# Performance work log

Hardware: AMD Instinct MI355X
Metric: run time of the kernel (lower is better)

The kernel has to match this reference:

```python
import jax, jax.numpy as jnp
import numpy as np

N = 8192
N_DIM = 7
N_WIDTH = 64


def setup_inputs() -> dict:
    key = jax.random.key(0)
    ks = jax.random.split(key, 12)
    scale = 0.05
    u = lambda k, shape: scale * (2.0 * jax.random.uniform(k, shape) - 1.0)
    # Linear params stored as (in, out) so forward uses x @ W + b (same math as torch Linear).
    lin = lambda k, fan_in, fan_out: (
        jax.random.uniform(jax.random.fold_in(k, 0), (fan_in, fan_out),
                           minval=-1.0, maxval=1.0) / np.sqrt(fan_in),
        jax.random.uniform(jax.random.fold_in(k, 1), (fan_out,),
                           minval=-1.0, maxval=1.0) / np.sqrt(fan_in),
    )
    W1, b1 = lin(ks[1], N_DIM, N_WIDTH)
    W2, b2 = lin(ks[2], N_WIDTH, N_WIDTH)
    Wl, bl = lin(ks[3], N_WIDTH, 1)
    return {
        "x": jax.random.normal(ks[0], (N, N_DIM), dtype=jnp.float32),
        "alpha": jax.random.uniform(ks[4], (1,)),          # Edges.alpha = 1 * rand(1)
        "W1": W1, "b1": b1, "wt1": u(ks[5], (N_WIDTH, N_WIDTH)), "bs1": u(ks[6], (1,)),
        "W2": W2, "b2": b2, "wt2": u(ks[7], (N_WIDTH, N_WIDTH)), "bs2": u(ks[8], (1,)),
        "Wl": Wl, "bl": bl,
    }


def _edges(x, alpha):
    eta, phi = x[:, 1], x[:, 2]
    deta = eta[:, None] - eta[None, :]                      # (n, n)
    dphi = jnp.abs(phi[:, None] - phi[None, :])
    dphi = jnp.where(dphi > jnp.pi, 2.0 * jnp.pi - dphi, dphi)
    dRdR = deta * deta + dphi * dphi
    A = jnp.exp(-alpha[0] * dRdR)
    return jax.nn.softmax(A, axis=1) + jnp.eye(x.shape[0], dtype=x.dtype)


def _gcn_layer(X, A, W, b, wt, bs):
    X = jax.nn.relu(X @ W + b)                              # embed + relu
    X = (A @ X) @ wt + bs[0]                                # aggregate + mix + scalar bias
    return jax.nn.relu(X)


def reference(x, alpha, W1, b1, wt1, bs1, W2, b2, wt2, bs2, Wl, bl):
    A = _edges(x, alpha)
    V = jax.nn.relu(_gcn_layer(x, A, W1, b1, wt1, bs1))
    V = jax.nn.relu(_gcn_layer(V, A, W2, b2, wt2, bs2))
    s = V.sum(axis=0)                                       # (n_width,)
    return jax.nn.sigmoid(s @ Wl + bl)                      # (1,)
```

## Files before the change

### kernel.cpp

```cpp
#include <hip/hip_runtime.h>
#include <math.h>

#define NN 8192
#define L2E 1.44269504088896340736f
#define TWO_PI 6.28318530717958647693f

typedef _Float16 h8 __attribute__((ext_vector_type(8)));
typedef _Float16 h4 __attribute__((ext_vector_type(4)));
typedef float f32x4 __attribute__((ext_vector_type(4)));
#define MFMA16(A, B, C) __builtin_amdgcn_mfma_f32_16x16x32_f16(A, B, C, 0, 0, 0)

#define GLD_LDS16(gsrc, ldst)                                          \
  __builtin_amdgcn_global_load_lds(                                    \
      (const __attribute__((address_space(1))) unsigned int*)(gsrc),   \
      (__attribute__((address_space(3))) unsigned int*)(ldst), 16, 0, 0)

union V8 { float4 v[2]; float f[8]; };

__global__ __launch_bounds__(256) void prep_kernel(
    const float* __restrict__ x, const float* __restrict__ alpha,
    const float* __restrict__ W1, const float* __restrict__ b1,
    float* __restrict__ eta_s, float* __restrict__ phi_s,
    float* __restrict__ H1, _Float16* __restrict__ HT1,
    float* __restrict__ svec)
{
  __shared__ float sW[448];
  __shared__ float sb[64];
  __shared__ float T[32][65];
  const int t = threadIdx.x;
  if (blockIdx.x == 0 && t < 64) svec[t] = 0.f;
  for (int k = t; k < 448; k += 256) sW[k] = W1[k];
  if (t < 64) sb[t] = b1[t];
  const float s = sqrtf(alpha[0] * L2E);
  const int i0 = blockIdx.x * 32;
  const int r = t >> 3, q = t & 7;
  const int i = i0 + r;
  float xv[7];
#pragma unroll
  for (int k = 0; k < 7; k++) xv[k] = x[i * 7 + k];
  if (q == 0) { eta_s[i] = xv[1] * s; phi_s[i] = xv[2] * s; }
  __syncthreads();
#pragma unroll
  for (int c = 0; c < 8; c++) {
    const int n = q * 8 + c;
    float hv = sb[n];
#pragma unroll
    for (int k = 0; k < 7; k++) hv = fmaf(xv[k], sW[k * 64 + n], hv);
    T[r][n] = fmaxf(hv, 0.f);
  }
  __syncthreads();
  for (int e = t; e < 2048; e += 256) H1[i0 * 64 + e] = T[e >> 6][e & 63];
  const int n = t >> 2, sg = (t & 3) * 8;
  h8 v;
#pragma unroll
  for (int ss = 0; ss < 8; ss++) v[ss] = (_Float16)T[sg + ss][n];
  *(h8*)(HT1 + (size_t)n * NN + i0 + sg) = v;
}

template <bool NEED_L>
__global__ __launch_bounds__(256, 4) void attn_pass(
    const float* __restrict__ eta_s, const float* __restrict__ phi_s,
    const _Float16* __restrict__ HT, const float* __restrict__ alpha,
    float* __restrict__ Ypart, float* __restrict__ lpart)
{
  __shared__ __align__(16) char smem[33792];
  _Float16* stage = (_Float16*)smem;
  const int tid = threadIdx.x;
  const int w = tid >> 6, lane = tid & 63, m = lane & 15, g = lane >> 4;
  const int tile = blockIdx.x >> 2, part = blockIdx.x & 3;
  const int i0 = tile << 5;
  const int jbase = part << 11;
  const float Cs = TWO_PI * sqrtf(alpha[0] * L2E);
  const float et0 = eta_s[i0 + m],      ph0 = phi_s[i0 + m];
  const float et1 = eta_s[i0 + 16 + m], ph1 = phi_s[i0 + 16 + m];

  const int r0 = tid >> 4, gq = tid & 15;
  const _Float16* sbase = HT + (size_t)r0 * NN + ((gq ^ r0) << 3) + jbase;

  f32x4 a00 = {0,0,0,0}, a01 = {0,0,0,0}, a02 = {0,0,0,0}, a03 = {0,0,0,0};
  f32x4 a10 = {0,0,0,0}, a11 = {0,0,0,0}, a12 = {0,0,0,0}, a13 = {0,0,0,0};
  float l0 = 0.f, l1 = 0.f;

  const float* ep = eta_s + jbase + (w << 5) + (g << 3);
  const float* pp = phi_s + jbase + (w << 5) + (g << 3);
  V8 E, P, En, Pn;
  E.v[0] = *(const float4*)ep;  E.v[1] = *(const float4*)(ep + 4);
  P.v[0] = *(const float4*)pp;  P.v[1] = *(const float4*)(pp + 4);
  En = E; Pn = P;

#pragma unroll
  for (int k = 0; k < 4; ++k)
    GLD_LDS16(sbase + (size_t)k * 16 * NN, stage + ((k * 256 + tid) << 3));
  __syncthreads();

  const int fs = ((m << 4) + (((w << 2) | g) ^ m)) << 3;

  union AF { h8 v; decltype(__builtin_amdgcn_cvt_pkrtz(0.f, 0.f)) p[4]; };

  for (int s = 0; s < 16; ++s) {
    _Float16* cur = stage + ((s & 1) << 13);
    if (s < 15) {
      _Float16* nxt = stage + (((s + 1) & 1) << 13);
      const _Float16* srcp = sbase + (s + 1) * 128;
#pragma unroll
      for (int k = 0; k < 4; ++k)
        GLD_LDS16(srcp + (size_t)k * 16 * NN, nxt + ((k * 256 + tid) << 3));
      En.v[0] = *(const float4*)(ep + 128); En.v[1] = *(const float4*)(ep + 132);
      Pn.v[0] = *(const float4*)(pp + 128); Pn.v[1] = *(const float4*)(pp + 132);
      ep += 128; pp += 128;
    }
    const h8 b0 = *(const h8*)(cur + fs);
    const h8 b1 = *(const h8*)(cur + 2048 + fs);
    const h8 b2 = *(const h8*)(cur + 4096 + fs);
    const h8 b3 = *(const h8*)(cur + 6144 + fs);

    AF af0, af1;
#pragma unroll
    for (int tt = 0; tt < 8; tt += 2) {
      float Pv[4];
#pragma unroll
      for (int u = 0; u < 2; ++u) {
        {
          const float dp = ph0 - P.f[tt + u];
          const float ad = fabsf(dp);
          const float wr = fminf(ad, Cs - ad);
          const float de = et0 - E.f[tt + u];
          const float r2 = fmaf(de, de, wr * wr);
          const float a  = __builtin_amdgcn_exp2f(-r2);
          const float pv = __builtin_amdgcn_exp2f(fmaf(a, L2E, -L2E));
          if constexpr (NEED_L) l0 += pv;
          Pv[u] = pv;
        }
        {
          const float dp = ph1 - P.f[tt + u];
          const float ad = fabsf(dp);
          const float wr = fminf(ad, Cs - ad);
          const float de = et1 - E.f[tt + u];
          const float r2 = fmaf(de, de, wr * wr);
          const float a  = __builtin_amdgcn_exp2f(-r2);
          const float pv = __builtin_amdgcn_exp2f(fmaf(a, L2E, -L2E));
          if constexpr (NEED_L) l1 += pv;
          Pv[2 + u] = pv;
        }
      }
      af0.p[tt >> 1] = __builtin_amdgcn_cvt_pkrtz(Pv[0], Pv[1]);
      af1.p[tt >> 1] = __builtin_amdgcn_cvt_pkrtz(Pv[2], Pv[3]);
    }
    a00 = MFMA16(af0.v, b0, a00); a01 = MFMA16(af0.v, b1, a01);
    a02 = MFMA16(af0.v, b2, a02); a03 = MFMA16(af0.v, b3, a03);
    a10 = MFMA16(af1.v, b0, a10); a11 = MFMA16(af1.v, b1, a11);
    a12 = MFMA16(af1.v, b2, a12); a13 = MFMA16(af1.v, b3, a13);
    E = En; P = Pn;
    __syncthreads();
  }

  typedef float Red2[32][66];
  Red2* red = (Red2*)smem;
  float* lredF = (float*)(smem + 32768);
  const int h = w >> 1;
  if ((w & 1) == 0) {
#pragma unroll
    for (int r = 0; r < 4; ++r) {
      red[h][g * 4 + r][m]      = a00[r]; red[h][g * 4 + r][16 + m] = a01[r];
      red[h][g * 4 + r][32 + m] = a02[r]; red[h][g * 4 + r][48 + m] = a03[r];
      red[h][16 + g * 4 + r][m]      = a10[r]; red[h][16 + g * 4 + r][16 + m] = a11[r];
      red[h][16 + g * 4 + r][32 + m] = a12[r]; red[h][16 + g * 4 + r][48 + m] = a13[r];
    }
    if constexpr (NEED_L) {
      lredF[h * 128 + g * 32 + m] = l0; lredF[h * 128 + g * 32 + 16 + m] = l1;
    }
  }
  __syncthreads();
  if (w & 1) {
#pragma unroll
    for (int r = 0; r < 4; ++r) {
      red[h][g * 4 + r][m]      += a00[r]; red[h][g * 4 + r][16 + m] += a01[r];
      red[h][g * 4 + r][32 + m] += a02[r]; red[h][g * 4 + r][48 + m] += a03[r];
      red[h][16 + g * 4 + r][m]      += a10[r]; red[h][16 + g * 4 + r][16 + m] += a11[r];
      red[h][16 + g * 4 + r][32 + m] += a12[r]; red[h][16 + g * 4 + r][48 + m] += a13[r];
    }
    if constexpr (NEED_L) {
      lredF[h * 128 + g * 32 + m] += l0; lredF[h * 128 + g * 32 + 16 + m] += l1;
    }
  }
  __syncthreads();
#pragma unroll
  for (int k = 0; k < 8; ++k) {
    const int e = tid + k * 256;
    Ypart[((size_t)part * NN + i0 + (e >> 6)) * 64 + (e & 63)] =
        red[0][e >> 6][e & 63] + red[1][e >> 6][e & 63];
  }
  if constexpr (NEED_L) {
    if (tid < 32) {
      float sv = 0.f;
#pragma unroll
      for (int hh = 0; hh < 2; ++hh)
#pragma unroll
        for (int gg = 0; gg < 4; ++gg) sv += lredF[hh * 128 + gg * 32 + tid];
      lpart[(size_t)part * NN + i0 + tid] = sv;
    }
  }
}

__global__ __launch_bounds__(256) void mid_kernel(
    const float* __restrict__ Yp, const float* __restrict__ lp,
    const float* __restrict__ H1, const float* __restrict__ wt1,
    const float* __restrict__ bs1, const float* __restrict__ W2,
    const float* __restrict__ b2, float* __restrict__ H2,
    _Float16* __restrict__ HT2)
{
  __shared__ float sA[64][68];
  __shared__ float sB[64][68];
  __shared__ float U[16][65];
  __shared__ float sb2v[64];
  const int t = threadIdx.x;
  for (int e = t; e < 4096; e += 256) {
    sA[e >> 6][e & 63] = wt1[e];
    sB[e >> 6][e & 63] = W2[e];
  }
  if (t < 64) sb2v[t] = b2[t];
  const float bsv = bs1[0];
  const int i0 = blockIdx.x * 16;
  const int r = t >> 4, q = t & 15;
  const int i = i0 + r;
  float l = 0.f;
#pragma unroll
  for (int p = 0; p < 4; ++p) l += lp[(size_t)p * NN + i];
  const float rl = 1.0f / l;
  f32x4 ya = {0, 0, 0, 0};
#pragma unroll
  for (int p = 0; p < 4; ++p)
    ya += *(const f32x4*)(Yp + ((size_t)p * NN + i) * 64 + q * 4);
  const f32x4 h1 = *(const f32x4*)(H1 + (size_t)i * 64 + q * 4);
#pragma unroll
  for (int c = 0; c < 4; ++c) U[r][q * 4 + c] = fmaf(ya[c], rl, h1[c]);
  __syncthreads();
  float z[4];
#pragma unroll
  for (int c = 0; c < 4; ++c) z[c] = bsv;
  for (int k = 0; k < 64; ++k) {
    const float uk = U[r][k];
    const f32x4 sa = *(const f32x4*)&sA[k][q * 4];
#pragma unroll
    for (int c = 0; c < 4; ++c) z[c] = fmaf(uk, sa[c], z[c]);
  }
  __syncthreads();
#pragma unroll
  for (int c = 0; c < 4; ++c) U[r][q * 4 + c] = fmaxf(z[c], 0.f);
  __syncthreads();
  float hv[4];
#pragma unroll
  for (int c = 0; c < 4; ++c) hv[c] = sb2v[q * 4 + c];
  for (int k = 0; k < 64; ++k) {
    const float uk = U[r][k];
    const f32x4 sb4 = *(const f32x4*)&sB[k][q * 4];
#pragma unroll
    for (int c = 0; c < 4; ++c) hv[c] = fmaf(uk, sb4[c], hv[c]);
  }
  __syncthreads();
#pragma unroll
  for (int c = 0; c < 4; ++c) U[r][q * 4 + c] = fmaxf(hv[c], 0.f);
  __syncthreads();
  for (int e = t; e < 1024; e += 256) H2[i0 * 64 + e] = U[e >> 6][e & 63];
  const int n = t >> 2, sg = (t & 3) * 4;
  h4 v;
#pragma unroll
  for (int ss = 0; ss < 4; ss++) v[ss] = (_Float16)U[sg + ss][n];
  *(h4*)(HT2 + (size_t)n * NN + i0 + sg) = v;
}

__global__ __launch_bounds__(256) void final_kernel(
    const float* __restrict__ Yp, const float* __restrict__ lp,
    const float* __restrict__ H2, const float* __restrict__ wt2,
    const float* __restrict__ bs2, float* __restrict__ svec)
{
  __shared__ float sA[64][68];
  __shared__ float U[16][65];
  __shared__ float cred[4][64];
  const int t = threadIdx.x;
  for (int e = t; e < 4096; e += 256) sA[e >> 6][e & 63] = wt2[e];
  const float bsv = bs2[0];
  const int i0 = blockIdx.x * 16;
  const int r = t >> 4, q = t & 15;
  const int i = i0 + r;
  float l = 0.f;
#pragma unroll
  for (int p = 0; p < 4; ++p) l += lp[(size_t)p * NN + i];
  const float rl = 1.0f / l;
  f32x4 ya = {0, 0, 0, 0};
#pragma unroll
  for (int p = 0; p < 4; ++p)
    ya += *(const f32x4*)(Yp + ((size_t)p * NN + i) * 64 + q * 4);
  const f32x4 h2 = *(const f32x4*)(H2 + (size_t)i * 64 + q * 4);
#pragma unroll
  for (int c = 0; c < 4; ++c) U[r][q * 4 + c] = fmaf(ya[c], rl, h2[c]);
  __syncthreads();
  float z[4];
#pragma unroll
  for (int c = 0; c < 4; ++c) z[c] = bsv;
  for (int k = 0; k < 64; ++k) {
    const float uk = U[r][k];
    const f32x4 sa = *(const f32x4*)&sA[k][q * 4];
#pragma unroll
    for (int c = 0; c < 4; ++c) z[c] = fmaf(uk, sa[c], z[c]);
  }
  __syncthreads();
#pragma unroll
  for (int c = 0; c < 4; ++c) U[r][q * 4 + c] = fmaxf(z[c], 0.f);
  __syncthreads();
  const int col = t & 63, rg = t >> 6;
  float ps = 0.f;
#pragma unroll
  for (int rr = 0; rr < 4; rr++) ps += U[rg * 4 + rr][col];
  cred[rg][col] = ps;
  __syncthreads();
  if (t < 64)
    atomicAdd(svec + t, cred[0][t] + cred[1][t] + cred[2][t] + cred[3][t]);
}

__global__ void out_kernel(const float* __restrict__ svec,
                           const float* __restrict__ Wl,
                           const float* __restrict__ bl,
                           float* __restrict__ out)
{
  const int t = threadIdx.x;
  float v = svec[t] * Wl[t];
#pragma unroll
  for (int off = 32; off > 0; off >>= 1) v += __shfl_down(v, off);
  if (t == 0) {
    const float logit = v + bl[0];
    out[0] = 1.0f / (1.0f + __builtin_amdgcn_exp2f(-logit * L2E));
  }
}

extern "C" void kernel_launch(void* const* d_in, const int* in_sizes, int n_in,
                              void* d_out, int out_size, void* d_ws,
                              size_t ws_size, hipStream_t stream)
{
  const float* x     = (const float*)d_in[0];
  const float* alpha = (const float*)d_in[1];
  const float* W1    = (const float*)d_in[2];
  const float* b1    = (const float*)d_in[3];
  const float* wt1   = (const float*)d_in[4];
  const float* bs1   = (const float*)d_in[5];
  const float* W2    = (const float*)d_in[6];
  const float* b2    = (const float*)d_in[7];
  const float* wt2   = (const float*)d_in[8];
  const float* bs2   = (const float*)d_in[9];
  const float* Wl    = (const float*)d_in[10];
  const float* bl    = (const float*)d_in[11];
  float* out = (float*)d_out;

  char* ws = (char*)d_ws;
  size_t off = 0;
  auto alloc = [&](size_t bytes) {
    void* p = ws + off;
    off = (off + bytes + 255) & ~(size_t)255;
    return p;
  };
  float* eta_s = (float*)alloc(NN * 4 + 256);
  float* phi_s = (float*)alloc(NN * 4 + 256);
  float* H1    = (float*)alloc((size_t)NN * 64 * 4);
  float* H2    = (float*)alloc((size_t)NN * 64 * 4);
  float* Ypart = (float*)alloc((size_t)4 * NN * 64 * 4);
  float* lpart = (float*)alloc((size_t)4 * NN * 4);
  _Float16* HT = (_Float16*)alloc((size_t)NN * 64 * 2 + 512);
  float* svec  = (float*)alloc(64 * 4);

  prep_kernel<<<256, 256, 0, stream>>>(x, alpha, W1, b1, eta_s, phi_s, H1, HT, svec);
  attn_pass<true><<<1024, 256, 0, stream>>>(eta_s, phi_s, HT, alpha, Ypart, lpart);
  mid_kernel<<<512, 256, 0, stream>>>(Ypart, lpart, H1, wt1, bs1, W2, b2, H2, HT);
  attn_pass<false><<<1024, 256, 0, stream>>>(eta_s, phi_s, HT, alpha, Ypart, nullptr);
  final_kernel<<<512, 256, 0, stream>>>(Ypart, lpart, H2, wt2, bs2, svec);
  out_kernel<<<1, 64, 0, stream>>>(svec, Wl, bl, out);
}
```

Measured before the change: 170.6 us.

## Fuse attention passes with per-row epilogues and drop split-K partials

Restructures each attention pass so a 512-thread block owns 16 rows across the full j range, reducing over its 8 waves in LDS instead of writing four Ypart partials. The mid/final dense layers and the final sigmoid (via a last-block atomic ticket) are folded into the same kernels, removing three launches and the partial-sum round-trip through global memory. The trade-offs are larger LDS use (64KB), half as many blocks per pass, and a serial epilogue tail inside each block.

```diff
diff --git a/kernel.cpp b/kernel.cpp
--- a/kernel.cpp
+++ b/kernel.cpp
@@ -6,7 +6,6 @@
 #define TWO_PI 6.28318530717958647693f
 
 typedef _Float16 h8 __attribute__((ext_vector_type(8)));
-typedef _Float16 h4 __attribute__((ext_vector_type(4)));
 typedef float f32x4 __attribute__((ext_vector_type(4)));
 #define MFMA16(A, B, C) __builtin_amdgcn_mfma_f32_16x16x32_f16(A, B, C, 0, 0, 0)
 
@@ -16,6 +15,7 @@
       (__attribute__((address_space(3))) unsigned int*)(ldst), 16, 0, 0)
 
 union V8 { float4 v[2]; float f[8]; };
+union AF { h8 v; decltype(__builtin_amdgcn_cvt_pkrtz(0.f, 0.f)) p[4]; };
 
 __global__ __launch_bounds__(256) void prep_kernel(
     const float* __restrict__ x, const float* __restrict__ alpha,
@@ -57,32 +57,46 @@
   *(h8*)(HT1 + (size_t)n * NN + i0 + sg) = v;
 }
 
-template <bool NEED_L>
-__global__ __launch_bounds__(256, 4) void attn_pass(
+template <int PASS>
+__global__ __launch_bounds__(512, 4) void fused_pass(
     const float* __restrict__ eta_s, const float* __restrict__ phi_s,
-    const _Float16* __restrict__ HT, const float* __restrict__ alpha,
-    float* __restrict__ Ypart, float* __restrict__ lpart)
+    const _Float16* __restrict__ HTin, const float* __restrict__ Hres,
+    const float* __restrict__ WA, const float* __restrict__ bsA,
+    const float* __restrict__ WB, const float* __restrict__ bB,
+    const float* __restrict__ alpha, float* __restrict__ lsum,
+    float* __restrict__ Hout, _Float16* __restrict__ HTout,
+    float* __restrict__ svec, const float* __restrict__ Wl,
+    const float* __restrict__ bl, float* __restrict__ out,
+    unsigned* __restrict__ bar)
 {
-  __shared__ __align__(16) char smem[33792];
+  __shared__ __align__(16) char smem[65536];
+  __shared__ unsigned last_ticket;
   _Float16* stage = (_Float16*)smem;
   const int tid = threadIdx.x;
   const int w = tid >> 6, lane = tid & 63, m = lane & 15, g = lane >> 4;
-  const int tile = blockIdx.x >> 2, part = blockIdx.x & 3;
-  const int i0 = tile << 5;
-  const int jbase = part << 11;
+  const int i0 = blockIdx.x << 4;
   const float Cs = TWO_PI * sqrtf(alpha[0] * L2E);
-  const float et0 = eta_s[i0 + m],      ph0 = phi_s[i0 + m];
-  const float et1 = eta_s[i0 + 16 + m], ph1 = phi_s[i0 + 16 + m];
-
-  const int r0 = tid >> 4, gq = tid & 15;
-  const _Float16* sbase = HT + (size_t)r0 * NN + ((gq ^ r0) << 3) + jbase;
-
-  f32x4 a00 = {0,0,0,0}, a01 = {0,0,0,0}, a02 = {0,0,0,0}, a03 = {0,0,0,0};
-  f32x4 a10 = {0,0,0,0}, a11 = {0,0,0,0}, a12 = {0,0,0,0}, a13 = {0,0,0,0};
-  float l0 = 0.f, l1 = 0.f;
-
-  const float* ep = eta_s + jbase + (w << 5) + (g << 3);
-  const float* pp = phi_s + jbase + (w << 5) + (g << 3);
+  const float et0 = eta_s[i0 + m], ph0 = phi_s[i0 + m];
+
+  const int rr = tid >> 5, gq = tid & 31;
+  const _Float16* sb4[4];
+#pragma unroll
+  for (int k = 0; k < 4; ++k) {
+    const int rowk = k * 16 + rr;
+    sb4[k] = HTin + (size_t)rowk * NN + ((gq ^ (rowk & 31)) << 3);
+  }
+  int fo[4];
+#pragma unroll
+  for (int c = 0; c < 4; ++c) {
+    const int row = c * 16 + m;
+    fo[c] = row * 256 + ((((w << 2) | g) ^ (row & 31)) << 3);
+  }
+
+  f32x4 a0 = {0,0,0,0}, a1 = {0,0,0,0}, a2 = {0,0,0,0}, a3 = {0,0,0,0};
+  float lacc = 0.f;
+
+  const float* ep = eta_s + (w << 5) + (g << 3);
+  const float* pp = phi_s + (w << 5) + (g << 3);
   V8 E, P, En, Pn;
   E.v[0] = *(const float4*)ep;  E.v[1] = *(const float4*)(ep + 4);
   P.v[0] = *(const float4*)pp;  P.v[1] = *(const float4*)(pp + 4);
@@ -90,246 +104,151 @@
 
 #pragma unroll
   for (int k = 0; k < 4; ++k)
-    GLD_LDS16(sbase + (size_t)k * 16 * NN, stage + ((k * 256 + tid) << 3));
-  __syncthreads();
-
-  const int fs = ((m << 4) + (((w << 2) | g) ^ m)) << 3;
-
-  union AF { h8 v; decltype(__builtin_amdgcn_cvt_pkrtz(0.f, 0.f)) p[4]; };
-
-  for (int s = 0; s < 16; ++s) {
-    _Float16* cur = stage + ((s & 1) << 13);
-    if (s < 15) {
-      _Float16* nxt = stage + (((s + 1) & 1) << 13);
-      const _Float16* srcp = sbase + (s + 1) * 128;
+    GLD_LDS16(sb4[k], stage + ((k * 512 + tid) << 3));
+  __syncthreads();
+
+  for (int s = 0; s < 32; ++s) {
+    _Float16* cur = stage + ((s & 1) << 14);
+    if (s < 31) {
+      _Float16* nxt = stage + (((s + 1) & 1) << 14);
+      const int joff = (s + 1) * 256;
 #pragma unroll
       for (int k = 0; k < 4; ++k)
-        GLD_LDS16(srcp + (size_t)k * 16 * NN, nxt + ((k * 256 + tid) << 3));
-      En.v[0] = *(const float4*)(ep + 128); En.v[1] = *(const float4*)(ep + 132);
-      Pn.v[0] = *(const float4*)(pp + 128); Pn.v[1] = *(const float4*)(pp + 132);
-      ep += 128; pp += 128;
-    }
-    const h8 b0 = *(const h8*)(cur + fs);
-    const h8 b1 = *(const h8*)(cur + 2048 + fs);
-    const h8 b2 = *(const h8*)(cur + 4096 + fs);
-    const h8 b3 = *(const h8*)(cur + 6144 + fs);
-
-    AF af0, af1;
+        GLD_LDS16(sb4[k] + joff, nxt + ((k * 512 + tid) << 3));
+      ep += 256; pp += 256;
+      En.v[0] = *(const float4*)ep;  En.v[1] = *(const float4*)(ep + 4);
+      Pn.v[0] = *(const float4*)pp;  Pn.v[1] = *(const float4*)(pp + 4);
+    }
+    const h8 b0 = *(const h8*)(cur + fo[0]);
+    const h8 b1 = *(const h8*)(cur + fo[1]);
+    const h8 b2 = *(const h8*)(cur + fo[2]);
+    const h8 b3 = *(const h8*)(cur + fo[3]);
+
+    AF af;
 #pragma unroll
     for (int tt = 0; tt < 8; tt += 2) {
-      float Pv[4];
+      float Pv[2];
 #pragma unroll
       for (int u = 0; u < 2; ++u) {
-        {
-          const float dp = ph0 - P.f[tt + u];
-          const float ad = fabsf(dp);
-          const float wr = fminf(ad, Cs - ad);
-          const float de = et0 - E.f[tt + u];
-          const float r2 = fmaf(de, de, wr * wr);
-          const float a  = __builtin_amdgcn_exp2f(-r2);
-          const float pv = __builtin_amdgcn_exp2f(fmaf(a, L2E, -L2E));
-          if constexpr (NEED_L) l0 += pv;
-          Pv[u] = pv;
-        }
-        {
-          const float dp = ph1 - P.f[tt + u];
-          const float ad = fabsf(dp);
-          const float wr = fminf(ad, Cs - ad);
-          const float de = et1 - E.f[tt + u];
-          const float r2 = fmaf(de, de, wr * wr);
-          const float a  = __builtin_amdgcn_exp2f(-r2);
-          const float pv = __builtin_amdgcn_exp2f(fmaf(a, L2E, -L2E));
-          if constexpr (NEED_L) l1 += pv;
-          Pv[2 + u] = pv;
+        const float dp = ph0 - P.f[tt + u];
+        const float ad = fabsf(dp);
+        const float wr = fminf(ad, Cs - ad);
+        const float de = et0 - E.f[tt + u];
+        const float r2 = fmaf(de, de, wr * wr);
+        const float a  = __builtin_amdgcn_exp2f(-r2);
+        const float pv = __builtin_amdgcn_exp2f(fmaf(a, L2E, -L2E));
+        if constexpr (PASS == 1) lacc += pv;
+        Pv[u] = pv;
+      }
+      af.p[tt >> 1] = __builtin_amdgcn_cvt_pkrtz(Pv[0], Pv[1]);
+    }
+    a0 = MFMA16(af.v, b0, a0); a1 = MFMA16(af.v, b1, a1);
+    a2 = MFMA16(af.v, b2, a2); a3 = MFMA16(af.v, b3, a3);
+    E = En; P = Pn;
+    __syncthreads();
+  }
+
+  float* RED  = (float*)smem;
+  float* LRED = (float*)(smem + 34816);
+  float* LROW = (float*)(smem + 36864);
+  float* UBUF = (float*)(smem + 37120);
+  float* ZBUF = (float*)(smem + 41728);
+
+#pragma unroll
+  for (int r = 0; r < 4; ++r) {
+    const int rowi = (w * 16 + g * 4 + r) * 68;
+    RED[rowi + m]      = a0[r];
+    RED[rowi + 16 + m] = a1[r];
+    RED[rowi + 32 + m] = a2[r];
+    RED[rowi + 48 + m] = a3[r];
+  }
+  if constexpr (PASS == 1) LRED[((w << 2) | g) * 16 + m] = lacc;
+  __syncthreads();
+
+  const int r  = tid >> 5;
+  const int c2 = (tid & 31) << 1;
+  float y0 = 0.f, y1 = 0.f;
+#pragma unroll
+  for (int q = 0; q < 8; ++q) {
+    y0 += RED[(q * 16 + r) * 68 + c2];
+    y1 += RED[(q * 16 + r) * 68 + c2 + 1];
+  }
+  const float2 hres = *(const float2*)(Hres + (size_t)(i0 + r) * 64 + c2);
+  if (tid < 16) {
+    float lv;
+    if constexpr (PASS == 1) {
+      lv = 0.f;
+#pragma unroll
+      for (int q = 0; q < 32; ++q) lv += LRED[q * 16 + tid];
+      lsum[i0 + tid] = lv;
+    } else {
+      lv = lsum[i0 + tid];
+    }
+    LROW[tid] = lv;
+  }
+  __syncthreads();
+
+  const float rl = 1.0f / LROW[r];
+  UBUF[r * 68 + c2]     = fmaf(y0, rl, hres.x);
+  UBUF[r * 68 + c2 + 1] = fmaf(y1, rl, hres.y);
+  __syncthreads();
+
+  float z0 = bsA[0], z1 = z0;
+  for (int k = 0; k < 64; ++k) {
+    const float uk = UBUF[r * 68 + k];
+    const float2 wv = *(const float2*)(WA + k * 64 + c2);
+    z0 = fmaf(uk, wv.x, z0);
+    z1 = fmaf(uk, wv.y, z1);
+  }
+  z0 = fmaxf(z0, 0.f); z1 = fmaxf(z1, 0.f);
+  ZBUF[r * 68 + c2]     = z0;
+  ZBUF[r * 68 + c2 + 1] = z1;
+  __syncthreads();
+
+  if constexpr (PASS == 1) {
+    float h0 = bB[c2], h1 = bB[c2 + 1];
+    for (int k = 0; k < 64; ++k) {
+      const float zk = ZBUF[r * 68 + k];
+      const float2 wv = *(const float2*)(WB + k * 64 + c2);
+      h0 = fmaf(zk, wv.x, h0);
+      h1 = fmaf(zk, wv.y, h1);
+    }
+    h0 = fmaxf(h0, 0.f); h1 = fmaxf(h1, 0.f);
+    float2 hw; hw.x = h0; hw.y = h1;
+    *(float2*)(Hout + (size_t)(i0 + r) * 64 + c2) = hw;
+    UBUF[r * 68 + c2]     = h0;
+    UBUF[r * 68 + c2 + 1] = h1;
+    __syncthreads();
+    const int n = tid >> 3, ri = (tid & 7) << 1;
+    union { _Float16 hh[2]; unsigned u; } pk;
+    pk.hh[0] = (_Float16)UBUF[ri * 68 + n];
+    pk.hh[1] = (_Float16)UBUF[(ri + 1) * 68 + n];
+    *(unsigned*)(HTout + (size_t)n * NN + i0 + ri) = pk.u;
+  } else {
+    if (tid < 64) {
+      float cs = 0.f;
+#pragma unroll
+      for (int rw = 0; rw < 16; ++rw) cs += ZBUF[rw * 68 + tid];
+      atomicAdd(svec + tid, cs);
+    }
+    __syncthreads();
+    if (tid == 0)
+      last_ticket = __hip_atomic_fetch_add(bar, 1u, __ATOMIC_RELAXED,
+                                           __HIP_MEMORY_SCOPE_AGENT);
+    __syncthreads();
+    if (last_ticket == gridDim.x - 1) {
+      if (tid == 0) __builtin_amdgcn_fence(__ATOMIC_ACQUIRE, "agent");
+      __syncthreads();
+      if (tid < 64) {
+        float v = svec[tid] * Wl[tid];
+#pragma unroll
+        for (int off = 32; off > 0; off >>= 1) v += __shfl_down(v, off);
+        if (tid == 0) {
+          const float logit = v + bl[0];
+          out[0] = 1.0f / (1.0f + __builtin_amdgcn_exp2f(-logit * L2E));
         }
       }
-      af0.p[tt >> 1] = __builtin_amdgcn_cvt_pkrtz(Pv[0], Pv[1]);
-      af1.p[tt >> 1] = __builtin_amdgcn_cvt_pkrtz(Pv[2], Pv[3]);
-    }
-    a00 = MFMA16(af0.v, b0, a00); a01 = MFMA16(af0.v, b1, a01);
-    a02 = MFMA16(af0.v, b2, a02); a03 = MFMA16(af0.v, b3, a03);
-    a10 = MFMA16(af1.v, b0, a10); a11 = MFMA16(af1.v, b1, a11);
-    a12 = MFMA16(af1.v, b2, a12); a13 = MFMA16(af1.v, b3, a13);
-    E = En; P = Pn;
-    __syncthreads();
-  }
-
-  typedef float Red2[32][66];
-  Red2* red = (Red2*)smem;
-  float* lredF = (float*)(smem + 32768);
-  const int h = w >> 1;
-  if ((w & 1) == 0) {
-#pragma unroll
-    for (int r = 0; r < 4; ++r) {
-      red[h][g * 4 + r][m]      = a00[r]; red[h][g * 4 + r][16 + m] = a01[r];
-      red[h][g * 4 + r][32 + m] = a02[r]; red[h][g * 4 + r][48 + m] = a03[r];
-      red[h][16 + g * 4 + r][m]      = a10[r]; red[h][16 + g * 4 + r][16 + m] = a11[r];
-      red[h][16 + g * 4 + r][32 + m] = a12[r]; red[h][16 + g * 4 + r][48 + m] = a13[r];
-    }
-    if constexpr (NEED_L) {
-      lredF[h * 128 + g * 32 + m] = l0; lredF[h * 128 + g * 32 + 16 + m] = l1;
-    }
-  }
-  __syncthreads();
-  if (w & 1) {
-#pragma unroll
-    for (int r = 0; r < 4; ++r) {
-      red[h][g * 4 + r][m]      += a00[r]; red[h][g * 4 + r][16 + m] += a01[r];
-      red[h][g * 4 + r][32 + m] += a02[r]; red[h][g * 4 + r][48 + m] += a03[r];
-      red[h][16 + g * 4 + r][m]      += a10[r]; red[h][16 + g * 4 + r][16 + m] += a11[r];
-      red[h][16 + g * 4 + r][32 + m] += a12[r]; red[h][16 + g * 4 + r][48 + m] += a13[r];
-    }
-    if constexpr (NEED_L) {
-      lredF[h * 128 + g * 32 + m] += l0; lredF[h * 128 + g * 32 + 16 + m] += l1;
-    }
-  }
-  __syncthreads();
-#pragma unroll
-  for (int k = 0; k < 8; ++k) {
-    const int e = tid + k * 256;
-    Ypart[((size_t)part * NN + i0 + (e >> 6)) * 64 + (e & 63)] =
-        red[0][e >> 6][e & 63] + red[1][e >> 6][e & 63];
-  }
-  if constexpr (NEED_L) {
-    if (tid < 32) {
-      float sv = 0.f;
-#pragma unroll
-      for (int hh = 0; hh < 2; ++hh)
-#pragma unroll
-        for (int gg = 0; gg < 4; ++gg) sv += lredF[hh * 128 + gg * 32 + tid];
-      lpart[(size_t)part * NN + i0 + tid] = sv;
-    }
-  }
-}
-
-__global__ __launch_bounds__(256) void mid_kernel(
-    const float* __restrict__ Yp, const float* __restrict__ lp,
-    const float* __restrict__ H1, const float* __restrict__ wt1,
-    const float* __restrict__ bs1, const float* __restrict__ W2,
-    const float* __restrict__ b2, float* __restrict__ H2,
-    _Float16* __restrict__ HT2)
-{
-  __shared__ float sA[64][68];
-  __shared__ float sB[64][68];
-  __shared__ float U[16][65];
-  __shared__ float sb2v[64];
-  const int t = threadIdx.x;
-  for (int e = t; e < 4096; e += 256) {
-    sA[e >> 6][e & 63] = wt1[e];
-    sB[e >> 6][e & 63] = W2[e];
-  }
-  if (t < 64) sb2v[t] = b2[t];
-  const float bsv = bs1[0];
-  const int i0 = blockIdx.x * 16;
-  const int r = t >> 4, q = t & 15;
-  const int i = i0 + r;
-  float l = 0.f;
-#pragma unroll
-  for (int p = 0; p < 4; ++p) l += lp[(size_t)p * NN + i];
-  const float rl = 1.0f / l;
-  f32x4 ya = {0, 0, 0, 0};
-#pragma unroll
-  for (int p = 0; p < 4; ++p)
-    ya += *(const f32x4*)(Yp + ((size_t)p * NN + i) * 64 + q * 4);
-  const f32x4 h1 = *(const f32x4*)(H1 + (size_t)i * 64 + q * 4);
-#pragma unroll
-  for (int c = 0; c < 4; ++c) U[r][q * 4 + c] = fmaf(ya[c], rl, h1[c]);
-  __syncthreads();
-  float z[4];
-#pragma unroll
-  for (int c = 0; c < 4; ++c) z[c] = bsv;
-  for (int k = 0; k < 64; ++k) {
-    const float uk = U[r][k];
-    const f32x4 sa = *(const f32x4*)&sA[k][q * 4];
-#pragma unroll
-    for (int c = 0; c < 4; ++c) z[c] = fmaf(uk, sa[c], z[c]);
-  }
-  __syncthreads();
-#pragma unroll
-  for (int c = 0; c < 4; ++c) U[r][q * 4 + c] = fmaxf(z[c], 0.f);
-  __syncthreads();
-  float hv[4];
-#pragma unroll
-  for (int c = 0; c < 4; ++c) hv[c] = sb2v[q * 4 + c];
-  for (int k = 0; k < 64; ++k) {
-    const float uk = U[r][k];
-    const f32x4 sb4 = *(const f32x4*)&sB[k][q * 4];
-#pragma unroll
-    for (int c = 0; c < 4; ++c) hv[c] = fmaf(uk, sb4[c], hv[c]);
-  }
-  __syncthreads();
-#pragma unroll
-  for (int c = 0; c < 4; ++c) U[r][q * 4 + c] = fmaxf(hv[c], 0.f);
-  __syncthreads();
-  for (int e = t; e < 1024; e += 256) H2[i0 * 64 + e] = U[e >> 6][e & 63];
-  const int n = t >> 2, sg = (t & 3) * 4;
-  h4 v;
-#pragma unroll
-  for (int ss = 0; ss < 4; ss++) v[ss] = (_Float16)U[sg + ss][n];
-  *(h4*)(HT2 + (size_t)n * NN + i0 + sg) = v;
-}
-
-__global__ __launch_bounds__(256) void final_kernel(
-    const float* __restrict__ Yp, const float* __restrict__ lp,
-    const float* __restrict__ H2, const float* __restrict__ wt2,
-    const float* __restrict__ bs2, float* __restrict__ svec)
-{
-  __shared__ float sA[64][68];
-  __shared__ float U[16][65];
-  __shared__ float cred[4][64];
-  const int t = threadIdx.x;
-  for (int e = t; e < 4096; e += 256) sA[e >> 6][e & 63] = wt2[e];
-  const float bsv = bs2[0];
-  const int i0 = blockIdx.x * 16;
-  const int r = t >> 4, q = t & 15;
-  const int i = i0 + r;
-  float l = 0.f;
-#pragma unroll
-  for (int p = 0; p < 4; ++p) l += lp[(size_t)p * NN + i];
-  const float rl = 1.0f / l;
-  f32x4 ya = {0, 0, 0, 0};
-#pragma unroll
-  for (int p = 0; p < 4; ++p)
-    ya += *(const f32x4*)(Yp + ((size_t)p * NN + i) * 64 + q * 4);
-  const f32x4 h2 = *(const f32x4*)(H2 + (size_t)i * 64 + q * 4);
-#pragma unroll
-  for (int c = 0; c < 4; ++c) U[r][q * 4 + c] = fmaf(ya[c], rl, h2[c]);
-  __syncthreads();
-  float z[4];
-#pragma unroll
-  for (int c = 0; c < 4; ++c) z[c] = bsv;
-  for (int k = 0; k < 64; ++k) {
-    const float uk = U[r][k];
-    const f32x4 sa = *(const f32x4*)&sA[k][q * 4];
-#pragma unroll
-    for (int c = 0; c < 4; ++c) z[c] = fmaf(uk, sa[c], z[c]);
-  }
-  __syncthreads();
-#pragma unroll
-  for (int c = 0; c < 4; ++c) U[r][q * 4 + c] = fmaxf(z[c], 0.f);
-  __syncthreads();
-  const int col = t & 63, rg = t >> 6;
-  float ps = 0.f;
-#pragma unroll
-  for (int rr = 0; rr < 4; rr++) ps += U[rg * 4 + rr][col];
-  cred[rg][col] = ps;
-  __syncthreads();
-  if (t < 64)
-    atomicAdd(svec + t, cred[0][t] + cred[1][t] + cred[2][t] + cred[3][t]);
-}
-
-__global__ void out_kernel(const float* __restrict__ svec,
-                           const float* __restrict__ Wl,
-                           const float* __restrict__ bl,
-                           float* __restrict__ out)
-{
-  const int t = threadIdx.x;
-  float v = svec[t] * Wl[t];
-#pragma unroll
-  for (int off = 32; off > 0; off >>= 1) v += __shfl_down(v, off);
-  if (t == 0) {
-    const float logit = v + bl[0];
-    out[0] = 1.0f / (1.0f + __builtin_amdgcn_exp2f(-logit * L2E));
+    }
   }
 }
 
@@ -358,19 +277,24 @@
     off = (off + bytes + 255) & ~(size_t)255;
     return p;
   };
-  float* eta_s = (float*)alloc(NN * 4 + 256);
-  float* phi_s = (float*)alloc(NN * 4 + 256);
-  float* H1    = (float*)alloc((size_t)NN * 64 * 4);
-  float* H2    = (float*)alloc((size_t)NN * 64 * 4);
-  float* Ypart = (float*)alloc((size_t)4 * NN * 64 * 4);
-  float* lpart = (float*)alloc((size_t)4 * NN * 4);
-  _Float16* HT = (_Float16*)alloc((size_t)NN * 64 * 2 + 512);
-  float* svec  = (float*)alloc(64 * 4);
-
-  prep_kernel<<<256, 256, 0, stream>>>(x, alpha, W1, b1, eta_s, phi_s, H1, HT, svec);
-  attn_pass<true><<<1024, 256, 0, stream>>>(eta_s, phi_s, HT, alpha, Ypart, lpart);
-  mid_kernel<<<512, 256, 0, stream>>>(Ypart, lpart, H1, wt1, bs1, W2, b2, H2, HT);
-  attn_pass<false><<<1024, 256, 0, stream>>>(eta_s, phi_s, HT, alpha, Ypart, nullptr);
-  final_kernel<<<512, 256, 0, stream>>>(Ypart, lpart, H2, wt2, bs2, svec);
-  out_kernel<<<1, 64, 0, stream>>>(svec, Wl, bl, out);
+  float* eta_s   = (float*)alloc(NN * 4 + 256);
+  float* phi_s   = (float*)alloc(NN * 4 + 256);
+  float* H1      = (float*)alloc((size_t)NN * 64 * 4);
+  float* H2      = (float*)alloc((size_t)NN * 64 * 4);
+  _Float16* HT1  = (_Float16*)alloc((size_t)NN * 64 * 2 + 512);
+  _Float16* HT2  = (_Float16*)alloc((size_t)NN * 64 * 2 + 512);
+  float* lsum    = (float*)alloc(NN * 4);
+  float* svec    = (float*)alloc(64 * 4);
+  unsigned* bar  = (unsigned*)alloc(256);
+
+  hipMemsetAsync(bar, 0, 256, stream);
+  prep_kernel<<<256, 256, 0, stream>>>(x, alpha, W1, b1, eta_s, phi_s, H1,
+                                       HT1, svec);
+  fused_pass<1><<<512, 512, 0, stream>>>(eta_s, phi_s, HT1, H1, wt1, bs1, W2,
+                                         b2, alpha, lsum, H2, HT2, nullptr,
+                                         nullptr, nullptr, nullptr, nullptr);
+  fused_pass<2><<<512, 512, 0, stream>>>(eta_s, phi_s, HT2, H2, wt2, bs2,
+                                         nullptr, nullptr, alpha, lsum,
+                                         nullptr, nullptr, svec, Wl, bl, out,
+                                         bar);
 }
```

Result: slower. 189.9 us (+11.3%).

## Fuse mid/final/out epilogues into attention passes via last-block tickets

Applied to the files above, without the earlier changes.

The separate mid, final and output kernels are removed. Each attention block now atomically accumulates its partial Y and row sums into global buffers. The last of the four split-K blocks per row tile, chosen by an atomic ticket, runs the per-tile MLP epilogue. The last tile overall in pass 2 computes the sigmoid output. This cuts six launches to three and drops the partial-buffer round trip, at the cost of float atomics, nondeterministic summation order, and a serial epilogue tail on the last-arriving blocks.

```diff
diff --git a/kernel.cpp b/kernel.cpp
--- a/kernel.cpp
+++ b/kernel.cpp
@@ -6,7 +6,6 @@
 #define TWO_PI 6.28318530717958647693f
 
 typedef _Float16 h8 __attribute__((ext_vector_type(8)));
-typedef _Float16 h4 __attribute__((ext_vector_type(4)));
 typedef float f32x4 __attribute__((ext_vector_type(4)));
 #define MFMA16(A, B, C) __builtin_amdgcn_mfma_f32_16x16x32_f16(A, B, C, 0, 0, 0)
 
@@ -16,23 +15,41 @@
       (__attribute__((address_space(3))) unsigned int*)(ldst), 16, 0, 0)
 
 union V8 { float4 v[2]; float f[8]; };
+union AF { h8 v; decltype(__builtin_amdgcn_cvt_pkrtz(0.f, 0.f)) p[4]; };
 
 __global__ __launch_bounds__(256) void prep_kernel(
     const float* __restrict__ x, const float* __restrict__ alpha,
     const float* __restrict__ W1, const float* __restrict__ b1,
     float* __restrict__ eta_s, float* __restrict__ phi_s,
     float* __restrict__ H1, _Float16* __restrict__ HT1,
-    float* __restrict__ svec)
+    float* __restrict__ lsum, float* __restrict__ Yacc1,
+    float* __restrict__ Yacc2, float* __restrict__ svec,
+    unsigned* __restrict__ tick1, unsigned* __restrict__ tick2,
+    unsigned* __restrict__ bar)
 {
   __shared__ float sW[448];
   __shared__ float sb[64];
   __shared__ float T[32][65];
   const int t = threadIdx.x;
-  if (blockIdx.x == 0 && t < 64) svec[t] = 0.f;
+  const int b = blockIdx.x;
+  {
+    const float4 z4 = {0.f, 0.f, 0.f, 0.f};
+#pragma unroll
+    for (int k = 0; k < 2; ++k) {
+      *(float4*)(Yacc1 + (size_t)b * 2048 + ((k * 256 + t) << 2)) = z4;
+      *(float4*)(Yacc2 + (size_t)b * 2048 + ((k * 256 + t) << 2)) = z4;
+    }
+    if (t < 32) lsum[b * 32 + t] = 0.f;
+    if (b == 0) {
+      tick1[t] = 0u; tick2[t] = 0u;
+      if (t < 64) svec[t] = 0.f;
+      if (t == 0) bar[0] = 0u;
+    }
+  }
   for (int k = t; k < 448; k += 256) sW[k] = W1[k];
   if (t < 64) sb[t] = b1[t];
   const float s = sqrtf(alpha[0] * L2E);
-  const int i0 = blockIdx.x * 32;
+  const int i0 = b * 32;
   const int r = t >> 3, q = t & 7;
   const int i = i0 + r;
   float xv[7];
@@ -57,13 +74,21 @@
   *(h8*)(HT1 + (size_t)n * NN + i0 + sg) = v;
 }
 
-template <bool NEED_L>
-__global__ __launch_bounds__(256, 4) void attn_pass(
+template <int PASS>
+__global__ __launch_bounds__(256, 4) void fused_pass(
     const float* __restrict__ eta_s, const float* __restrict__ phi_s,
-    const _Float16* __restrict__ HT, const float* __restrict__ alpha,
-    float* __restrict__ Ypart, float* __restrict__ lpart)
+    const _Float16* __restrict__ HTin, const float* __restrict__ Hres,
+    const float* __restrict__ WA, const float* __restrict__ bsA,
+    const float* __restrict__ WB, const float* __restrict__ bB,
+    const float* __restrict__ alpha, float* __restrict__ lsum,
+    float* __restrict__ Yacc, float* __restrict__ Hout,
+    _Float16* __restrict__ HTout, float* __restrict__ svec,
+    const float* __restrict__ Wl, const float* __restrict__ bl,
+    float* __restrict__ out, unsigned* __restrict__ tick,
+    unsigned* __restrict__ bar)
 {
   __shared__ __align__(16) char smem[33792];
+  __shared__ unsigned last;
   _Float16* stage = (_Float16*)smem;
   const int tid = threadIdx.x;
   const int w = tid >> 6, lane = tid & 63, m = lane & 15, g = lane >> 4;
@@ -75,7 +100,7 @@
   const float et1 = eta_s[i0 + 16 + m], ph1 = phi_s[i0 + 16 + m];
 
   const int r0 = tid >> 4, gq = tid & 15;
-  const _Float16* sbase = HT + (size_t)r0 * NN + ((gq ^ r0) << 3) + jbase;
+  const _Float16* sbase = HTin + (size_t)r0 * NN + ((gq ^ r0) << 3) + jbase;
 
   f32x4 a00 = {0,0,0,0}, a01 = {0,0,0,0}, a02 = {0,0,0,0}, a03 = {0,0,0,0};
   f32x4 a10 = {0,0,0,0}, a11 = {0,0,0,0}, a12 = {0,0,0,0}, a13 = {0,0,0,0};
@@ -94,8 +119,6 @@
   __syncthreads();
 
   const int fs = ((m << 4) + (((w << 2) | g) ^ m)) << 3;
-
-  union AF { h8 v; decltype(__builtin_amdgcn_cvt_pkrtz(0.f, 0.f)) p[4]; };
 
   for (int s = 0; s < 16; ++s) {
     _Float16* cur = stage + ((s & 1) << 13);
@@ -128,7 +151,7 @@
           const float r2 = fmaf(de, de, wr * wr);
           const float a  = __builtin_amdgcn_exp2f(-r2);
           const float pv = __builtin_amdgcn_exp2f(fmaf(a, L2E, -L2E));
-          if constexpr (NEED_L) l0 += pv;
+          if constexpr (PASS == 1) l0 += pv;
           Pv[u] = pv;
         }
         {
@@ -139,7 +162,7 @@
           const float r2 = fmaf(de, de, wr * wr);
           const float a  = __builtin_amdgcn_exp2f(-r2);
           const float pv = __builtin_amdgcn_exp2f(fmaf(a, L2E, -L2E));
-          if constexpr (NEED_L) l1 += pv;
+          if constexpr (PASS == 1) l1 += pv;
           Pv[2 + u] = pv;
         }
       }
@@ -166,7 +189,7 @@
       red[h][16 + g * 4 + r][m]      = a10[r]; red[h][16 + g * 4 + r][16 + m] = a11[r];
       red[h][16 + g * 4 + r][32 + m] = a12[r]; red[h][16 + g * 4 + r][48 + m] = a13[r];
     }
-    if constexpr (NEED_L) {
+    if constexpr (PASS == 1) {
       lredF[h * 128 + g * 32 + m] = l0; lredF[h * 128 + g * 32 + 16 + m] = l1;
     }
   }
@@ -179,157 +202,135 @@
       red[h][16 + g * 4 + r][m]      += a10[r]; red[h][16 + g * 4 + r][16 + m] += a11[r];
       red[h][16 + g * 4 + r][32 + m] += a12[r]; red[h][16 + g * 4 + r][48 + m] += a13[r];
     }
-    if constexpr (NEED_L) {
+    if constexpr (PASS == 1) {
       lredF[h * 128 + g * 32 + m] += l0; lredF[h * 128 + g * 32 + 16 + m] += l1;
     }
   }
   __syncthreads();
+
 #pragma unroll
   for (int k = 0; k < 8; ++k) {
-    const int e = tid + k * 256;
-    Ypart[((size_t)part * NN + i0 + (e >> 6)) * 64 + (e & 63)] =
-        red[0][e >> 6][e & 63] + red[1][e >> 6][e & 63];
-  }
-  if constexpr (NEED_L) {
+    const int e = tid + (k << 8);
+    atomicAdd(Yacc + (((size_t)(i0 + (e >> 6))) << 6) + (e & 63),
+              red[0][e >> 6][e & 63] + red[1][e >> 6][e & 63]);
+  }
+  if constexpr (PASS == 1) {
     if (tid < 32) {
       float sv = 0.f;
 #pragma unroll
       for (int hh = 0; hh < 2; ++hh)
 #pragma unroll
         for (int gg = 0; gg < 4; ++gg) sv += lredF[hh * 128 + gg * 32 + tid];
-      lpart[(size_t)part * NN + i0 + tid] = sv;
-    }
-  }
-}
-
-__global__ __launch_bounds__(256) void mid_kernel(
-    const float* __restrict__ Yp, const float* __restrict__ lp,
-    const float* __restrict__ H1, const float* __restrict__ wt1,
-    const float* __restrict__ bs1, const float* __restrict__ W2,
-    const float* __restrict__ b2, float* __restrict__ H2,
-    _Float16* __restrict__ HT2)
-{
-  __shared__ float sA[64][68];
-  __shared__ float sB[64][68];
-  __shared__ float U[16][65];
-  __shared__ float sb2v[64];
-  const int t = threadIdx.x;
-  for (int e = t; e < 4096; e += 256) {
-    sA[e >> 6][e & 63] = wt1[e];
-    sB[e >> 6][e & 63] = W2[e];
-  }
-  if (t < 64) sb2v[t] = b2[t];
-  const float bsv = bs1[0];
-  const int i0 = blockIdx.x * 16;
-  const int r = t >> 4, q = t & 15;
-  const int i = i0 + r;
-  float l = 0.f;
-#pragma unroll
-  for (int p = 0; p < 4; ++p) l += lp[(size_t)p * NN + i];
-  const float rl = 1.0f / l;
-  f32x4 ya = {0, 0, 0, 0};
-#pragma unroll
-  for (int p = 0; p < 4; ++p)
-    ya += *(const f32x4*)(Yp + ((size_t)p * NN + i) * 64 + q * 4);
-  const f32x4 h1 = *(const f32x4*)(H1 + (size_t)i * 64 + q * 4);
-#pragma unroll
-  for (int c = 0; c < 4; ++c) U[r][q * 4 + c] = fmaf(ya[c], rl, h1[c]);
-  __syncthreads();
-  float z[4];
-#pragma unroll
-  for (int c = 0; c < 4; ++c) z[c] = bsv;
+      atomicAdd(lsum + i0 + tid, sv);
+    }
+  }
+  __syncthreads();
+  if (tid == 0)
+    last = __hip_atomic_fetch_add(tick + tile, 1u, __ATOMIC_RELAXED,
+                                  __HIP_MEMORY_SCOPE_AGENT);
+  __syncthreads();
+  if (last != 3) return;
+  if (tid == 0) __builtin_amdgcn_fence(__ATOMIC_ACQUIRE, "agent");
+  __syncthreads();
+
+  float* UBUF = (float*)smem;
+  float* ZBUF = (float*)(smem + 8704);
+  float* LROW = (float*)(smem + 17408);
+  const int r  = tid >> 3;
+  const int c0 = (tid & 7) << 3;
+  if (tid < 32) LROW[tid] = lsum[i0 + tid];
+  __syncthreads();
+  const float rl = 1.0f / LROW[r];
+  {
+    const size_t rowb = ((size_t)(i0 + r)) << 6;
+    const f32x4 ya = *(const f32x4*)(Yacc + rowb + c0);
+    const f32x4 yb = *(const f32x4*)(Yacc + rowb + c0 + 4);
+    const f32x4 ha = *(const f32x4*)(Hres + rowb + c0);
+    const f32x4 hb = *(const f32x4*)(Hres + rowb + c0 + 4);
+#pragma unroll
+    for (int c = 0; c < 4; ++c) {
+      UBUF[r * 68 + c0 + c]     = fmaf(ya[c], rl, ha[c]);
+      UBUF[r * 68 + c0 + 4 + c] = fmaf(yb[c], rl, hb[c]);
+    }
+  }
+  __syncthreads();
+  float z[8];
+  const float bz = bsA[0];
+#pragma unroll
+  for (int c = 0; c < 8; ++c) z[c] = bz;
   for (int k = 0; k < 64; ++k) {
-    const float uk = U[r][k];
-    const f32x4 sa = *(const f32x4*)&sA[k][q * 4];
-#pragma unroll
-    for (int c = 0; c < 4; ++c) z[c] = fmaf(uk, sa[c], z[c]);
-  }
-  __syncthreads();
-#pragma unroll
-  for (int c = 0; c < 4; ++c) U[r][q * 4 + c] = fmaxf(z[c], 0.f);
-  __syncthreads();
-  float hv[4];
-#pragma unroll
-  for (int c = 0; c < 4; ++c) hv[c] = sb2v[q * 4 + c];
-  for (int k = 0; k < 64; ++k) {
-    const float uk = U[r][k];
-    const f32x4 sb4 = *(const f32x4*)&sB[k][q * 4];
-#pragma unroll
-    for (int c = 0; c < 4; ++c) hv[c] = fmaf(uk, sb4[c], hv[c]);
-  }
-  __syncthreads();
-#pragma unroll
-  for (int c = 0; c < 4; ++c) U[r][q * 4 + c] = fmaxf(hv[c], 0.f);
-  __syncthreads();
-  for (int e = t; e < 1024; e += 256) H2[i0 * 64 + e] = U[e >> 6][e & 63];
-  const int n = t >> 2, sg = (t & 3) * 4;
-  h4 v;
-#pragma unroll
-  for (int ss = 0; ss < 4; ss++) v[ss] = (_Float16)U[sg + ss][n];
-  *(h4*)(HT2 + (size_t)n * NN + i0 + sg) = v;
-}
-
-__global__ __launch_bounds__(256) void final_kernel(
-    const float* __restrict__ Yp, const float* __restrict__ lp,
-    const float* __restrict__ H2, const float* __restrict__ wt2,
-    const float* __restrict__ bs2, float* __restrict__ svec)
-{
-  __shared__ float sA[64][68];
-  __shared__ float U[16][65];
-  __shared__ float cred[4][64];
-  const int t = threadIdx.x;
-  for (int e = t; e < 4096; e += 256) sA[e >> 6][e & 63] = wt2[e];
-  const float bsv = bs2[0];
-  const int i0 = blockIdx.x * 16;
-  const int r = t >> 4, q = t & 15;
-  const int i = i0 + r;
-  float l = 0.f;
-#pragma unroll
-  for (int p = 0; p < 4; ++p) l += lp[(size_t)p * NN + i];
-  const float rl = 1.0f / l;
-  f32x4 ya = {0, 0, 0, 0};
-#pragma unroll
-  for (int p = 0; p < 4; ++p)
-    ya += *(const f32x4*)(Yp + ((size_t)p * NN + i) * 64 + q * 4);
-  const f32x4 h2 = *(const f32x4*)(H2 + (size_t)i * 64 + q * 4);
-#pragma unroll
-  for (int c = 0; c < 4; ++c) U[r][q * 4 + c] = fmaf(ya[c], rl, h2[c]);
-  __syncthreads();
-  float z[4];
-#pragma unroll
-  for (int c = 0; c < 4; ++c) z[c] = bsv;
-  for (int k = 0; k < 64; ++k) {
-    const float uk = U[r][k];
-    const f32x4 sa = *(const f32x4*)&sA[k][q * 4];
-#pragma unroll
-    for (int c = 0; c < 4; ++c) z[c] = fmaf(uk, sa[c], z[c]);
-  }
-  __syncthreads();
-#pragma unroll
-  for (int c = 0; c < 4; ++c) U[r][q * 4 + c] = fmaxf(z[c], 0.f);
-  __syncthreads();
-  const int col = t & 63, rg = t >> 6;
-  float ps = 0.f;
-#pragma unroll
-  for (int rr = 0; rr < 4; rr++) ps += U[rg * 4 + rr][col];
-  cred[rg][col] = ps;
-  __syncthreads();
-  if (t < 64)
-    atomicAdd(svec + t, cred[0][t] + cred[1][t] + cred[2][t] + cred[3][t]);
-}
-
-__global__ void out_kernel(const float* __restrict__ svec,
-                           const float* __restrict__ Wl,
-                           const float* __restrict__ bl,
-                           float* __restrict__ out)
-{
-  const int t = threadIdx.x;
-  float v = svec[t] * Wl[t];
-#pragma unroll
-  for (int off = 32; off > 0; off >>= 1) v += __shfl_down(v, off);
-  if (t == 0) {
-    const float logit = v + bl[0];
-    out[0] = 1.0f / (1.0f + __builtin_amdgcn_exp2f(-logit * L2E));
+    const float uk = UBUF[r * 68 + k];
+    const f32x4 wa = *(const f32x4*)(WA + (k << 6) + c0);
+    const f32x4 wb = *(const f32x4*)(WA + (k << 6) + c0 + 4);
+#pragma unroll
+    for (int c = 0; c < 4; ++c) {
+      z[c]     = fmaf(uk, wa[c], z[c]);
+      z[4 + c] = fmaf(uk, wb[c], z[4 + c]);
+    }
+  }
+#pragma unroll
+  for (int c = 0; c < 8; ++c) ZBUF[r * 68 + c0 + c] = fmaxf(z[c], 0.f);
+  __syncthreads();
+
+  if constexpr (PASS == 1) {
+    float hh[8];
+#pragma unroll
+    for (int c = 0; c < 8; ++c) hh[c] = bB[c0 + c];
+    for (int k = 0; k < 64; ++k) {
+      const float zk = ZBUF[r * 68 + k];
+      const f32x4 wa = *(const f32x4*)(WB + (k << 6) + c0);
+      const f32x4 wb = *(const f32x4*)(WB + (k << 6) + c0 + 4);
+#pragma unroll
+      for (int c = 0; c < 4; ++c) {
+        hh[c]     = fmaf(zk, wa[c], hh[c]);
+        hh[4 + c] = fmaf(zk, wb[c], hh[4 + c]);
+      }
+    }
+    f32x4 ha, hb2;
+#pragma unroll
+    for (int c = 0; c < 4; ++c) {
+      ha[c]  = fmaxf(hh[c], 0.f);
+      hb2[c] = fmaxf(hh[4 + c], 0.f);
+    }
+    const size_t rowb = ((size_t)(i0 + r)) << 6;
+    *(f32x4*)(Hout + rowb + c0)     = ha;
+    *(f32x4*)(Hout + rowb + c0 + 4) = hb2;
+#pragma unroll
+    for (int c = 0; c < 4; ++c) {
+      UBUF[r * 68 + c0 + c]     = ha[c];
+      UBUF[r * 68 + c0 + 4 + c] = hb2[c];
+    }
+    __syncthreads();
+    const int n = tid >> 2, ri = (tid & 3) << 3;
+    h8 v;
+#pragma unroll
+    for (int ss = 0; ss < 8; ++ss) v[ss] = (_Float16)UBUF[(ri + ss) * 68 + n];
+    *(h8*)(HTout + (size_t)n * NN + i0 + ri) = v;
+  } else {
+    if (tid < 64) {
+      float cs = 0.f;
+#pragma unroll
+      for (int rw = 0; rw < 32; ++rw) cs += ZBUF[rw * 68 + tid];
+      atomicAdd(svec + tid, cs);
+    }
+    __syncthreads();
+    if (tid == 0)
+      last = __hip_atomic_fetch_add(bar, 1u, __ATOMIC_RELAXED,
+                                    __HIP_MEMORY_SCOPE_AGENT);
+    __syncthreads();
+    if (last == (gridDim.x >> 2) - 1) {
+      if (tid == 0) __builtin_amdgcn_fence(__ATOMIC_ACQUIRE, "agent");
+      __syncthreads();
+      if (tid < 64) {
+        float v = svec[tid] * Wl[tid];
+#pragma unroll
+        for (int off = 32; off > 0; off >>= 1) v += __shfl_down(v, off);
+        if (tid == 0) {
+          const float logit = v + bl[0];
+          out[0] = 1.0f / (1.0f + __builtin_amdgcn_exp2f(-logit * L2E));
+        }
+      }
+    }
   }
 }
 
@@ -358,19 +359,29 @@
     off = (off + bytes + 255) & ~(size_t)255;
     return p;
   };
-  float* eta_s = (float*)alloc(NN * 4 + 256);
-  float* phi_s = (float*)alloc(NN * 4 + 256);
-  float* H1    = (float*)alloc((size_t)NN * 64 * 4);
-  float* H2    = (float*)alloc((size_t)NN * 64 * 4);
-  float* Ypart = (float*)alloc((size_t)4 * NN * 64 * 4);
-  float* lpart = (float*)alloc((size_t)4 * NN * 4);
-  _Float16* HT = (_Float16*)alloc((size_t)NN * 64 * 2 + 512);
-  float* svec  = (float*)alloc(64 * 4);
-
-  prep_kernel<<<256, 256, 0, stream>>>(x, alpha, W1, b1, eta_s, phi_s, H1, HT, svec);
-  attn_pass<true><<<1024, 256, 0, stream>>>(eta_s, phi_s, HT, alpha, Ypart, lpart);
-  mid_kernel<<<512, 256, 0, stream>>>(Ypart, lpart, H1, wt1, bs1, W2, b2, H2, HT);
-  attn_pass<false><<<1024, 256, 0, stream>>>(eta_s, phi_s, HT, alpha, Ypart, nullptr);
-  final_kernel<<<512, 256, 0, stream>>>(Ypart, lpart, H2, wt2, bs2, svec);
-  out_kernel<<<1, 64, 0, stream>>>(svec, Wl, bl, out);
+  float* eta_s   = (float*)alloc(NN * 4 + 512);
+  float* phi_s   = (float*)alloc(NN * 4 + 512);
+  float* H1      = (float*)alloc((size_t)NN * 64 * 4);
+  float* H2      = (float*)alloc((size_t)NN * 64 * 4);
+  _Float16* HT1  = (_Float16*)alloc((size_t)NN * 64 * 2 + 512);
+  _Float16* HT2  = (_Float16*)alloc((size_t)NN * 64 * 2 + 512);
+  float* Yacc1   = (float*)alloc((size_t)NN * 64 * 4);
+  float* Yacc2   = (float*)alloc((size_t)NN * 64 * 4);
+  float* lsum    = (float*)alloc(NN * 4);
+  float* svec    = (float*)alloc(64 * 4);
+  unsigned* tick1 = (unsigned*)alloc(256 * 4);
+  unsigned* tick2 = (unsigned*)alloc(256 * 4);
+  unsigned* bar   = (unsigned*)alloc(256);
+
+  prep_kernel<<<256, 256, 0, stream>>>(x, alpha, W1, b1, eta_s, phi_s, H1,
+                                       HT1, lsum, Yacc1, Yacc2, svec, tick1,
+                                       tick2, bar);
+  fused_pass<1><<<1024, 256, 0, stream>>>(eta_s, phi_s, HT1, H1, wt1, bs1,
+                                          W2, b2, alpha, lsum, Yacc1, H2,
+                                          HT2, nullptr, nullptr, nullptr,
+                                          nullptr, tick1, nullptr);
+  fused_pass<2><<<1024, 256, 0, stream>>>(eta_s, phi_s, HT2, H2, wt2, bs2,
+                                          nullptr, nullptr, alpha, lsum,
+                                          Yacc2, nullptr, nullptr, svec, Wl,
+                                          bl, out, tick2, bar);
 }
```

After: 194.8 us. +14.2%, slower.
